# Optimization experiments

Measured on AMD Instinct MI355X. Metric: run time of the kernel, lower is better.

## Reference

```python
import jax, jax.numpy as jnp
import numpy as np
from jax import lax

DIVISOR = 2.0


def setup_inputs() -> dict:
    key = jax.random.key(0)
    k1, k2, k3, k4 = jax.random.split(key, 4)
    x = jax.random.normal(k1, (128, 8, 32, 32, 32), dtype=jnp.float32)
    conv_weight = jax.random.normal(k2, (16, 8, 3, 3, 3), dtype=jnp.float32) * 0.1
    conv_bias = jax.random.normal(k3, (16,), dtype=jnp.float32) * 0.1
    bias = jax.random.normal(k4, (16, 1, 1, 1), dtype=jnp.float32) * 0.1
    return {"x": x, "conv_weight": conv_weight, "conv_bias": conv_bias, "bias": bias}


def reference(x, conv_weight, conv_bias, bias):
    # Conv3d, stride 1, no padding: [B,8,32,32,32] -> [B,16,30,30,30]
    y = lax.conv_general_dilated(
        x, conv_weight,
        window_strides=(1, 1, 1), padding='VALID',
        dimension_numbers=('NCDHW', 'OIDHW', 'NCDHW'))
    y = y + conv_bias[None, :, None, None, None]
    # divide by scalar divisor
    y = y / DIVISOR
    # MaxPool3d kernel=stride=2: [B,16,30,30,30] -> [B,16,15,15,15]
    y = lax.reduce_window(
        y, -jnp.inf, lax.max,
        window_dimensions=(1, 1, 2, 2, 2),
        window_strides=(1, 1, 2, 2, 2),
        padding='VALID')
    # AdaptiveAvgPool3d((1,1,1)): global mean over D,H,W -> [B,16,1,1,1]
    y = jnp.mean(y, axis=(2, 3, 4), keepdims=True)
    # bias add (bias shape [16,1,1,1] broadcasts over batch)
    y = y + bias
    # sum over channel dim (dim=1) -> [B,1,1,1]
    return jnp.sum(y, axis=1)
```

## Files before the change

### kernel.cpp

```cpp
#include <hip/hip_runtime.h>


using short8 = __attribute__((ext_vector_type(8))) short;
using f32x4  = __attribute__((ext_vector_type(4))) float;

__device__ __forceinline__ unsigned short f2bf(float f) {
  unsigned u = __float_as_uint(f);
  return (unsigned short)((u + 0x7FFFu + ((u >> 16) & 1u)) >> 16);
}

__global__ __launch_bounds__(256) void prep_w(const float* __restrict__ cw,
                                              short* __restrict__ Bp) {
  int i = threadIdx.x + blockIdx.x * 256;
  if (i >= 576) return;
  int g = i >> 6, l = i & 63;
  int co = l & 15, kw = l >> 4;
  int kd = g / 3, kh = g % 3;
  short8 o;
#pragma unroll
  for (int j = 0; j < 8; ++j) {
    float v = (kw < 3) ? cw[(co * 8 + j) * 27 + kd * 9 + kh * 3 + kw] : 0.0f;
    o[j] = (short)f2bf(v);
  }
  *(short8*)(Bp + (size_t)i * 8) = o;
}

__global__ __launch_bounds__(512, 4) void conv_mfma(const float* __restrict__ x,
                                                    const short* __restrict__ Bp,
                                                    float* __restrict__ partial) {
  __shared__ __align__(16) short xs[32768];
  __shared__ float red[8];
  const int flat = blockIdx.x;
  const int swz = (flat & 7) * 240 + (flat >> 3);
  const int pd = swz % 15, b = swz / 15;
  const int t = threadIdx.x;
  const int d0 = pd * 2;
  char* xc = (char*)xs;

  {
    const float* xb = x + (size_t)b * 262144;
    for (int s = t; s < 1024; s += 512) {
      const int d = s >> 8, h = (s >> 3) & 31, wc = s & 7;
      float4 va[8];
#pragma unroll
      for (int ci = 0; ci < 8; ++ci)
        va[ci] = *(const float4*)(x + (size_t)b * 262144 + (size_t)ci * 32768 +
                                  (d0 + d) * 1024 + h * 32 + wc * 4);
      (void)xb;
#pragma unroll
      for (int wi = 0; wi < 4; ++wi) {
        const int w = wc * 4 + wi;
        short8 o;
#pragma unroll
        for (int ci = 0; ci < 8; ++ci)
          o[ci] = (short)f2bf(((const float*)&va[ci])[wi]);
        const int byte = ((d * 1024 + h * 32 + w) * 16) ^ (((w >> 3) & 3) << 4);
        *(short8*)(xc + byte) = o;
      }
    }
  }

  const int lane = t & 63, wv = t >> 6;

  short8 Bw[9];
#pragma unroll
  for (int g = 0; g < 9; ++g)
    Bw[g] = *(const short8*)(Bp + ((size_t)g * 64 + lane) * 8);

  const int m = lane & 15, tg = lane >> 4;
  const int w0 = m + tg;
  int w1 = m + 16 + tg;
  if (w1 > 31) w1 = 31;
  const int wb0 = (w0 * 16) ^ (((w0 >> 3) & 3) << 4);
  const int wb1 = (w1 * 16) ^ (((w1 >> 3) & 3) << 4);

  __syncthreads();

  float sum = 0.0f;
  for (int tid = wv; tid < 30; tid += 8) {
    const int q = tid >> 1, c = tid & 1;
    const int base = (c ? wb1 : wb0) + q * 1024;
    f32x4 cc[2][2] = {};
#pragma unroll
    for (int p = 0; p < 4; ++p) {
#pragma unroll
      for (int r = 0; r < 4; ++r) {
        const short8 a = *(const short8*)(xc + base + p * 16384 + r * 512);
        if (p < 3 && r < 3)
          cc[0][0] = __builtin_amdgcn_mfma_f32_16x16x32_bf16(a, Bw[p * 3 + r], cc[0][0], 0, 0, 0);
        if (p < 3 && r > 0)
          cc[0][1] = __builtin_amdgcn_mfma_f32_16x16x32_bf16(a, Bw[p * 3 + r - 1], cc[0][1], 0, 0, 0);
        if (p > 0 && r < 3)
          cc[1][0] = __builtin_amdgcn_mfma_f32_16x16x32_bf16(a, Bw[(p - 1) * 3 + r], cc[1][0], 0, 0, 0);
        if (p > 0 && r > 0)
          cc[1][1] = __builtin_amdgcn_mfma_f32_16x16x32_bf16(a, Bw[(p - 1) * 3 + r - 1], cc[1][1], 0, 0, 0);
      }
    }
#pragma unroll
    for (int p2 = 0; p2 < 2; ++p2) {
      float v = fmaxf(fmaxf(fmaxf(cc[0][0][2 * p2], cc[0][0][2 * p2 + 1]),
                            fmaxf(cc[0][1][2 * p2], cc[0][1][2 * p2 + 1])),
                      fmaxf(fmaxf(cc[1][0][2 * p2], cc[1][0][2 * p2 + 1]),
                            fmaxf(cc[1][1][2 * p2], cc[1][1][2 * p2 + 1])));
      const bool inval = (c == 1) && (tg == 3) && (p2 == 1);
      sum += inval ? 0.0f : v;
    }
  }

#pragma unroll
  for (int off = 32; off; off >>= 1) sum += __shfl_down(sum, off);
  if (lane == 0) red[wv] = sum;
  __syncthreads();
  if (t == 0) {
    float s2 = 0.0f;
#pragma unroll
    for (int wvi = 0; wvi < 8; ++wvi) s2 += red[wvi];
    partial[b * 15 + pd] = s2;
  }
}

__global__ __launch_bounds__(64) void finalize(const float* __restrict__ partial,
                                               const float* __restrict__ cb,
                                               const float* __restrict__ bias,
                                               float* __restrict__ out) {
  const int b = blockIdx.x, t = threadIdx.x;
  float s = (t < 15) ? partial[b * 15 + t] : 0.0f;
#pragma unroll
  for (int off = 32; off; off >>= 1) s += __shfl_down(s, off);
  if (t == 0) {
    float k = 0.0f;
#pragma unroll
    for (int c = 0; c < 16; ++c) k += cb[c] * 0.5f + bias[c];
    out[b] = s * (1.0f / 6750.0f) + k;
  }
}

extern "C" void kernel_launch(void* const* d_in, const int* in_sizes, int n_in,
                              void* d_out, int out_size, void* d_ws, size_t ws_size,
                              hipStream_t stream) {
  const float* x    = (const float*)d_in[0];
  const float* cw   = (const float*)d_in[1];
  const float* cb   = (const float*)d_in[2];
  const float* bias = (const float*)d_in[3];
  float* out = (float*)d_out;

  short* Bp      = (short*)d_ws;
  float* partial = (float*)((char*)d_ws + 16384);

  prep_w<<<3, 256, 0, stream>>>(cw, Bp);
  conv_mfma<<<1920, 512, 0, stream>>>(x, Bp, partial);
  finalize<<<128, 64, 0, stream>>>(partial, cb, bias, out);
}
```

Measured before the change: 45.42 us.

## Stream depth planes through a ring buffer with 32x32 MFMA and register prefetch

Each block now handles half of one batch sample's depth range instead of a single pooled depth slab. It keeps a 6-plane LDS ring buffer and prefetches the next two input planes into registers while MFMA work runs, so neighbouring slabs no longer reload overlapping planes. The convolution moves to 32x32x16 bf16 MFMAs, with the weights repacked so both output depths of a pool pair are computed together. Only 256 blocks are launched, so load balance and occupancy (launch bounds lowered to 2) become risks, along with more register pressure from 18 weight fragments.

```diff
diff --git a/kernel.cpp b/kernel.cpp
--- a/kernel.cpp
+++ b/kernel.cpp
@@ -2,7 +2,7 @@
 
 
 using short8 = __attribute__((ext_vector_type(8))) short;
-using f32x4  = __attribute__((ext_vector_type(4))) float;
+using f32x16 = __attribute__((ext_vector_type(16))) float;
 
 __device__ __forceinline__ unsigned short f2bf(float f) {
   unsigned u = __float_as_uint(f);
@@ -12,99 +12,145 @@
 __global__ __launch_bounds__(256) void prep_w(const float* __restrict__ cw,
                                               short* __restrict__ Bp) {
   int i = threadIdx.x + blockIdx.x * 256;
-  if (i >= 576) return;
+  if (i >= 1152) return;
   int g = i >> 6, l = i & 63;
-  int co = l & 15, kw = l >> 4;
-  int kd = g / 3, kh = g % 3;
+  int pb2 = g / 9, kh = (g / 3) % 3, kw = g % 3;
+  int col = l & 31, koff = l >> 5;
+  int co = col & 15, od = col >> 4;
+  int kd = 2 * pb2 + koff - od;
   short8 o;
 #pragma unroll
   for (int j = 0; j < 8; ++j) {
-    float v = (kw < 3) ? cw[(co * 8 + j) * 27 + kd * 9 + kh * 3 + kw] : 0.0f;
+    float v = (kd >= 0 && kd <= 2) ? cw[(co * 8 + j) * 27 + kd * 9 + kh * 3 + kw] : 0.0f;
     o[j] = (short)f2bf(v);
   }
   *(short8*)(Bp + (size_t)i * 8) = o;
 }
 
-__global__ __launch_bounds__(512, 4) void conv_mfma(const float* __restrict__ x,
+__global__ __launch_bounds__(512, 2) void conv_mfma(const float* __restrict__ x,
                                                     const short* __restrict__ Bp,
                                                     float* __restrict__ partial) {
-  __shared__ __align__(16) short xs[32768];
+  __shared__ __align__(16) char lds[6 * 16384];
   __shared__ float red[8];
-  const int flat = blockIdx.x;
-  const int swz = (flat & 7) * 240 + (flat >> 3);
-  const int pd = swz % 15, b = swz / 15;
-  const int t = threadIdx.x;
-  const int d0 = pd * 2;
-  char* xc = (char*)xs;
+  const int blk = blockIdx.x;
+  const int b = blk >> 1, dh = blk & 1;
+  const int t = threadIdx.x, lane = t & 63, wv = t >> 6;
+  const int pd0 = dh ? 7 : 0;
+  const int nst = dh ? 8 : 7;
+  const int plane0 = 2 * pd0;
+  const float* xb = x + (size_t)b * 262144;
 
-  {
-    const float* xb = x + (size_t)b * 262144;
-    for (int s = t; s < 1024; s += 512) {
-      const int d = s >> 8, h = (s >> 3) & 31, wc = s & 7;
-      float4 va[8];
+  const int ow = lane & 31, koff = lane >> 5, hi = lane >> 5;
+  int wbv[3];
 #pragma unroll
-      for (int ci = 0; ci < 8; ++ci)
-        va[ci] = *(const float4*)(x + (size_t)b * 262144 + (size_t)ci * 32768 +
-                                  (d0 + d) * 1024 + h * 32 + wc * 4);
-      (void)xb;
-#pragma unroll
-      for (int wi = 0; wi < 4; ++wi) {
-        const int w = wc * 4 + wi;
-        short8 o;
-#pragma unroll
-        for (int ci = 0; ci < 8; ++ci)
-          o[ci] = (short)f2bf(((const float*)&va[ci])[wi]);
-        const int byte = ((d * 1024 + h * 32 + w) * 16) ^ (((w >> 3) & 3) << 4);
-        *(short8*)(xc + byte) = o;
-      }
-    }
+  for (int kw = 0; kw < 3; ++kw) {
+    int w = ow + kw; if (w > 31) w = 31;
+    wbv[kw] = (w * 16) ^ (((w >> 3) & 3) << 4);
   }
 
-  const int lane = t & 63, wv = t >> 6;
+  const int sh = t >> 4, swq = (t >> 1) & 7, sch = t & 1;
+  const float* gbase = xb + (size_t)(sch * 4) * 32768 + sh * 32 + swq * 4;
 
-  short8 Bw[9];
+  auto loadSite = [&](int d, float4& v0, float4& v1, float4& v2, float4& v3) {
+    const float* gp = gbase + d * 1024;
+    v0 = *(const float4*)(gp);
+    v1 = *(const float4*)(gp + 32768);
+    v2 = *(const float4*)(gp + 65536);
+    v3 = *(const float4*)(gp + 98304);
+  };
+  auto storeSite = [&](int d, const float4& v0, const float4& v1, const float4& v2,
+                       const float4& v3) {
+    char* sb = lds + (d % 6) * 16384 + sh * 512 + sch * 8;
+    const float* a0 = (const float*)&v0; const float* a1 = (const float*)&v1;
+    const float* a2 = (const float*)&v2; const float* a3 = (const float*)&v3;
 #pragma unroll
-  for (int g = 0; g < 9; ++g)
+    for (int j = 0; j < 4; ++j) {
+      int w = swq * 4 + j;
+      int wbyte = (w * 16) ^ (((w >> 3) & 3) << 4);
+      uint2 val;
+      val.x = (unsigned)f2bf(a0[j]) | ((unsigned)f2bf(a1[j]) << 16);
+      val.y = (unsigned)f2bf(a2[j]) | ((unsigned)f2bf(a3[j]) << 16);
+      *(uint2*)(sb + wbyte) = val;
+    }
+  };
+
+#pragma unroll
+  for (int pr = 0; pr < 4; ++pr) {
+    float4 v0, v1, v2, v3;
+    loadSite(plane0 + pr, v0, v1, v2, v3);
+    storeSite(plane0 + pr, v0, v1, v2, v3);
+  }
+
+  short8 Bw[18];
+#pragma unroll
+  for (int g = 0; g < 18; ++g)
     Bw[g] = *(const short8*)(Bp + ((size_t)g * 64 + lane) * 8);
-
-  const int m = lane & 15, tg = lane >> 4;
-  const int w0 = m + tg;
-  int w1 = m + 16 + tg;
-  if (w1 > 31) w1 = 31;
-  const int wb0 = (w0 * 16) ^ (((w0 >> 3) & 3) << 4);
-  const int wb1 = (w1 * 16) ^ (((w1 >> 3) & 3) << 4);
 
   __syncthreads();
 
   float sum = 0.0f;
-  for (int tid = wv; tid < 30; tid += 8) {
-    const int q = tid >> 1, c = tid & 1;
-    const int base = (c ? wb1 : wb0) + q * 1024;
-    f32x4 cc[2][2] = {};
+  for (int st = 0; st < nst; ++st) {
+    const int pd = pd0 + st;
+    const bool more = (st < nst - 1);
+    const int dpair = 2 * pd + 4;
+
+    int b6 = (2 * pd) % 6;
+    int s0 = b6 + koff; if (s0 >= 6) s0 -= 6;
+    int s1 = b6 + 2 + koff; if (s1 >= 6) s1 -= 6;
+    char* lp0 = lds + s0 * 16384;
+    char* lp1 = lds + s1 * 16384;
+
+    auto chunk = [&](int q) {
+      const int oh0 = 2 * q;
+      short8 fS[4][6];
 #pragma unroll
-    for (int p = 0; p < 4; ++p) {
+      for (int j = 0; j < 4; ++j) {
+        char* r0 = lp0 + (oh0 + j) * 512;
+        char* r1 = lp1 + (oh0 + j) * 512;
 #pragma unroll
-      for (int r = 0; r < 4; ++r) {
-        const short8 a = *(const short8*)(xc + base + p * 16384 + r * 512);
-        if (p < 3 && r < 3)
-          cc[0][0] = __builtin_amdgcn_mfma_f32_16x16x32_bf16(a, Bw[p * 3 + r], cc[0][0], 0, 0, 0);
-        if (p < 3 && r > 0)
-          cc[0][1] = __builtin_amdgcn_mfma_f32_16x16x32_bf16(a, Bw[p * 3 + r - 1], cc[0][1], 0, 0, 0);
-        if (p > 0 && r < 3)
-          cc[1][0] = __builtin_amdgcn_mfma_f32_16x16x32_bf16(a, Bw[(p - 1) * 3 + r], cc[1][0], 0, 0, 0);
-        if (p > 0 && r > 0)
-          cc[1][1] = __builtin_amdgcn_mfma_f32_16x16x32_bf16(a, Bw[(p - 1) * 3 + r - 1], cc[1][1], 0, 0, 0);
+        for (int kw = 0; kw < 3; ++kw) {
+          fS[j][kw]     = *(const short8*)(r0 + wbv[kw]);
+          fS[j][3 + kw] = *(const short8*)(r1 + wbv[kw]);
+        }
       }
+      f32x16 C[2] = {};
+#pragma unroll
+      for (int pb2 = 0; pb2 < 2; ++pb2)
+#pragma unroll
+        for (int kh = 0; kh < 3; ++kh)
+#pragma unroll
+          for (int kw = 0; kw < 3; ++kw) {
+            const int fi = pb2 * 3 + kw;
+            const int g = (pb2 * 3 + kh) * 3 + kw;
+            C[0] = __builtin_amdgcn_mfma_f32_32x32x16_bf16(fS[kh][fi], Bw[g], C[0], 0, 0, 0);
+            C[1] = __builtin_amdgcn_mfma_f32_32x32x16_bf16(fS[kh + 1][fi], Bw[g], C[1], 0, 0, 0);
+          }
+      float part = 0.0f;
+#pragma unroll
+      for (int i = 0; i < 8; ++i) {
+        float v = fmaxf(fmaxf(C[0][2 * i], C[0][2 * i + 1]),
+                        fmaxf(C[1][2 * i], C[1][2 * i + 1]));
+        v = fmaxf(v, __shfl_xor(v, 16));
+        if (((lane & 31) < 16) && !(hi == 1 && i == 7)) part += v;
+      }
+      sum += part;
+    };
+
+    float4 v0, v1, v2, v3;
+    if (more) loadSite(dpair, v0, v1, v2, v3);
+
+    chunk(wv);
+
+    if (more) {
+      storeSite(dpair, v0, v1, v2, v3);
+      loadSite(dpair + 1, v0, v1, v2, v3);
     }
-#pragma unroll
-    for (int p2 = 0; p2 < 2; ++p2) {
-      float v = fmaxf(fmaxf(fmaxf(cc[0][0][2 * p2], cc[0][0][2 * p2 + 1]),
-                            fmaxf(cc[0][1][2 * p2], cc[0][1][2 * p2 + 1])),
-                      fmaxf(fmaxf(cc[1][0][2 * p2], cc[1][0][2 * p2 + 1]),
-                            fmaxf(cc[1][1][2 * p2], cc[1][1][2 * p2 + 1])));
-      const bool inval = (c == 1) && (tg == 3) && (p2 == 1);
-      sum += inval ? 0.0f : v;
-    }
+
+    if (wv < 7) chunk(wv + 8);
+
+    if (more) storeSite(dpair + 1, v0, v1, v2, v3);
+
+    __syncthreads();
   }
 
 #pragma unroll
@@ -114,25 +160,21 @@
   if (t == 0) {
     float s2 = 0.0f;
 #pragma unroll
-    for (int wvi = 0; wvi < 8; ++wvi) s2 += red[wvi];
-    partial[b * 15 + pd] = s2;
+    for (int i = 0; i < 8; ++i) s2 += red[i];
+    partial[blk] = s2;
   }
 }
 
-__global__ __launch_bounds__(64) void finalize(const float* __restrict__ partial,
-                                               const float* __restrict__ cb,
-                                               const float* __restrict__ bias,
-                                               float* __restrict__ out) {
-  const int b = blockIdx.x, t = threadIdx.x;
-  float s = (t < 15) ? partial[b * 15 + t] : 0.0f;
+__global__ __launch_bounds__(128) void finalize(const float* __restrict__ partial,
+                                                const float* __restrict__ cb,
+                                                const float* __restrict__ bias,
+                                                float* __restrict__ out) {
+  int b = threadIdx.x;
+  if (b >= 128) return;
+  float k = 0.0f;
 #pragma unroll
-  for (int off = 32; off; off >>= 1) s += __shfl_down(s, off);
-  if (t == 0) {
-    float k = 0.0f;
-#pragma unroll
-    for (int c = 0; c < 16; ++c) k += cb[c] * 0.5f + bias[c];
-    out[b] = s * (1.0f / 6750.0f) + k;
-  }
+  for (int c = 0; c < 16; ++c) k += cb[c] * 0.5f + bias[c];
+  out[b] = (partial[2 * b] + partial[2 * b + 1]) * (1.0f / 6750.0f) + k;
 }
 
 extern "C" void kernel_launch(void* const* d_in, const int* in_sizes, int n_in,
@@ -145,9 +187,9 @@
   float* out = (float*)d_out;
 
   short* Bp      = (short*)d_ws;
-  float* partial = (float*)((char*)d_ws + 16384);
+  float* partial = (float*)((char*)d_ws + 32768);
 
-  prep_w<<<3, 256, 0, stream>>>(cw, Bp);
-  conv_mfma<<<1920, 512, 0, stream>>>(x, Bp, partial);
-  finalize<<<128, 64, 0, stream>>>(partial, cb, bias, out);
+  prep_w<<<5, 256, 0, stream>>>(cw, Bp);
+  conv_mfma<<<256, 512, 0, stream>>>(x, Bp, partial);
+  finalize<<<1, 128, 0, stream>>>(partial, cb, bias, out);
 }
```

Result: slower. 50.14 us (+10.4%).

## Split conv blocks along H into halves with smaller LDS tiles and 256 threads

Applied to the files above, without the earlier changes.

Each workgroup now handles half of the H range (18 input rows with halo) for one depth slab, with 256 threads and about 36KB of LDS instead of 512 threads and 64KB. The grid doubles to 3840 blocks and the partial sums are indexed per half. The aim is higher occupancy and more blocks to hide load latency. In exchange, the two-row halo is loaded twice, raising global reads by roughly 12%.

```diff
diff --git a/kernel.cpp b/kernel.cpp
--- a/kernel.cpp
+++ b/kernel.cpp
@@ -25,42 +25,39 @@
   *(short8*)(Bp + (size_t)i * 8) = o;
 }
 
-__global__ __launch_bounds__(512, 4) void conv_mfma(const float* __restrict__ x,
+__global__ __launch_bounds__(256, 4) void conv_mfma(const float* __restrict__ x,
                                                     const short* __restrict__ Bp,
                                                     float* __restrict__ partial) {
-  __shared__ __align__(16) short xs[32768];
-  __shared__ float red[8];
+  __shared__ __align__(16) char lds[4 * 18 * 512];
+  __shared__ float red[4];
+
   const int flat = blockIdx.x;
-  const int swz = (flat & 7) * 240 + (flat >> 3);
-  const int pd = swz % 15, b = swz / 15;
-  const int t = threadIdx.x;
-  const int d0 = pd * 2;
-  char* xc = (char*)xs;
+  const int xcd = flat & 7, idx = flat >> 3;
+  const int b   = xcd * 16 + idx / 30;
+  const int r30 = idx % 30;
+  const int pd  = r30 >> 1, hh = r30 & 1;
+  const int t = threadIdx.x, lane = t & 63, wv = t >> 6;
+  const int d0  = pd * 2;
+  const int hbs = hh ? 14 : 0;
+  const float* xb = x + (size_t)b * 262144;
 
-  {
-    const float* xb = x + (size_t)b * 262144;
-    for (int s = t; s < 1024; s += 512) {
-      const int d = s >> 8, h = (s >> 3) & 31, wc = s & 7;
-      float4 va[8];
+  for (int s = t; s < 576; s += 256) {
+    const int d = s / 144, rem = s % 144;
+    const int hr = rem >> 3, wc = rem & 7;
+    const float* gp = xb + (d0 + d) * 1024 + (hbs + hr) * 32 + wc * 4;
+    float4 va[8];
 #pragma unroll
-      for (int ci = 0; ci < 8; ++ci)
-        va[ci] = *(const float4*)(x + (size_t)b * 262144 + (size_t)ci * 32768 +
-                                  (d0 + d) * 1024 + h * 32 + wc * 4);
-      (void)xb;
+    for (int ci = 0; ci < 8; ++ci) va[ci] = *(const float4*)(gp + ci * 32768);
+    char* rowp = lds + (d * 18 + hr) * 512;
 #pragma unroll
-      for (int wi = 0; wi < 4; ++wi) {
-        const int w = wc * 4 + wi;
-        short8 o;
+    for (int wi = 0; wi < 4; ++wi) {
+      const int w = wc * 4 + wi;
+      short8 o;
 #pragma unroll
-        for (int ci = 0; ci < 8; ++ci)
-          o[ci] = (short)f2bf(((const float*)&va[ci])[wi]);
-        const int byte = ((d * 1024 + h * 32 + w) * 16) ^ (((w >> 3) & 3) << 4);
-        *(short8*)(xc + byte) = o;
-      }
+      for (int ci = 0; ci < 8; ++ci) o[ci] = (short)f2bf(((const float*)&va[ci])[wi]);
+      *(short8*)(rowp + ((w * 16) ^ (((w >> 3) & 3) << 4))) = o;
     }
   }
-
-  const int lane = t & 63, wv = t >> 6;
 
   short8 Bw[9];
 #pragma unroll
@@ -69,31 +66,32 @@
 
   const int m = lane & 15, tg = lane >> 4;
   const int w0 = m + tg;
-  int w1 = m + 16 + tg;
-  if (w1 > 31) w1 = 31;
+  int w1 = m + 16 + tg; if (w1 > 31) w1 = 31;
   const int wb0 = (w0 * 16) ^ (((w0 >> 3) & 3) << 4);
   const int wb1 = (w1 * 16) ^ (((w1 >> 3) & 3) << 4);
 
   __syncthreads();
 
+  const int ntasks = hh ? 14 : 16;
+  const int rowoff = hh ? 2 : 0;
   float sum = 0.0f;
-  for (int tid = wv; tid < 30; tid += 8) {
-    const int q = tid >> 1, c = tid & 1;
-    const int base = (c ? wb1 : wb0) + q * 1024;
+  for (int tid = wv; tid < ntasks; tid += 4) {
+    const int ql = tid >> 1, c = tid & 1;
+    const int base = (c ? wb1 : wb0) + (2 * ql + rowoff) * 512;
     f32x4 cc[2][2] = {};
 #pragma unroll
     for (int p = 0; p < 4; ++p) {
 #pragma unroll
-      for (int r = 0; r < 4; ++r) {
-        const short8 a = *(const short8*)(xc + base + p * 16384 + r * 512);
-        if (p < 3 && r < 3)
-          cc[0][0] = __builtin_amdgcn_mfma_f32_16x16x32_bf16(a, Bw[p * 3 + r], cc[0][0], 0, 0, 0);
-        if (p < 3 && r > 0)
-          cc[0][1] = __builtin_amdgcn_mfma_f32_16x16x32_bf16(a, Bw[p * 3 + r - 1], cc[0][1], 0, 0, 0);
-        if (p > 0 && r < 3)
-          cc[1][0] = __builtin_amdgcn_mfma_f32_16x16x32_bf16(a, Bw[(p - 1) * 3 + r], cc[1][0], 0, 0, 0);
-        if (p > 0 && r > 0)
-          cc[1][1] = __builtin_amdgcn_mfma_f32_16x16x32_bf16(a, Bw[(p - 1) * 3 + r - 1], cc[1][1], 0, 0, 0);
+      for (int rr = 0; rr < 4; ++rr) {
+        const short8 a = *(const short8*)(lds + base + p * 9216 + rr * 512);
+        if (p < 3 && rr < 3)
+          cc[0][0] = __builtin_amdgcn_mfma_f32_16x16x32_bf16(a, Bw[p * 3 + rr], cc[0][0], 0, 0, 0);
+        if (p < 3 && rr > 0)
+          cc[0][1] = __builtin_amdgcn_mfma_f32_16x16x32_bf16(a, Bw[p * 3 + rr - 1], cc[0][1], 0, 0, 0);
+        if (p > 0 && rr < 3)
+          cc[1][0] = __builtin_amdgcn_mfma_f32_16x16x32_bf16(a, Bw[(p - 1) * 3 + rr], cc[1][0], 0, 0, 0);
+        if (p > 0 && rr > 0)
+          cc[1][1] = __builtin_amdgcn_mfma_f32_16x16x32_bf16(a, Bw[(p - 1) * 3 + rr - 1], cc[1][1], 0, 0, 0);
       }
     }
 #pragma unroll
@@ -111,12 +109,8 @@
   for (int off = 32; off; off >>= 1) sum += __shfl_down(sum, off);
   if (lane == 0) red[wv] = sum;
   __syncthreads();
-  if (t == 0) {
-    float s2 = 0.0f;
-#pragma unroll
-    for (int wvi = 0; wvi < 8; ++wvi) s2 += red[wvi];
-    partial[b * 15 + pd] = s2;
-  }
+  if (t == 0)
+    partial[b * 30 + pd * 2 + hh] = red[0] + red[1] + red[2] + red[3];
 }
 
 __global__ __launch_bounds__(64) void finalize(const float* __restrict__ partial,
@@ -124,7 +118,7 @@
                                                const float* __restrict__ bias,
                                                float* __restrict__ out) {
   const int b = blockIdx.x, t = threadIdx.x;
-  float s = (t < 15) ? partial[b * 15 + t] : 0.0f;
+  float s = (t < 30) ? partial[b * 30 + t] : 0.0f;
 #pragma unroll
   for (int off = 32; off; off >>= 1) s += __shfl_down(s, off);
   if (t == 0) {
@@ -145,9 +139,9 @@
   float* out = (float*)d_out;
 
   short* Bp      = (short*)d_ws;
-  float* partial = (float*)((char*)d_ws + 16384);
+  float* partial = (float*)((char*)d_ws + 32768);
 
   prep_w<<<3, 256, 0, stream>>>(cw, Bp);
-  conv_mfma<<<1920, 512, 0, stream>>>(x, Bp, partial);
+  conv_mfma<<<3840, 256, 0, stream>>>(x, Bp, partial);
   finalize<<<128, 64, 0, stream>>>(partial, cb, bias, out);
 }
```

Result: slower. 46.61 us (+2.6%).
